# Kernel optimization log

Measured on AMD Instinct MI355X. Metric: run time of the kernel, lower is better.

The kernel has to match this reference:

```python
import jax, jax.numpy as jnp
import numpy as np

B, Q, P, H, W = 4, 64, 32, 512, 512
IDENTITY_ALPHA_EPSILON = 0.001


def setup_inputs() -> dict:
    key = jax.random.key(0)
    k1, k2, k3, k4, k5 = jax.random.split(key, 5)
    patch_alpha = jax.random.uniform(k1, (B, Q, P, P), dtype=jnp.float32)            # sigmoid-like in [0,1]
    centers = jax.random.uniform(k2, (B, Q, 2), dtype=jnp.float32) * 2.0 - 1.0       # tanh range
    depth = jax.random.uniform(k3, (B, Q, 1), dtype=jnp.float32) * 5.0               # sigmoid*5
    sizes = jax.random.uniform(k4, (B, Q, 2), dtype=jnp.float32) * 0.08 + 0.015      # sigmoid*0.08+0.015
    depth_scale = jax.random.uniform(k5, (B, Q, 1), dtype=jnp.float32)
    return {"patch_alpha": patch_alpha, "centers": centers, "depth": depth,
            "sizes": sizes, "depth_scale": depth_scale}


def _grid_sample_bilinear_zeros(img, ix, iy):
    # img: [N,h,w]; ix,iy: pixel coords [N,H,W]; bilinear, zero padding, align_corners=True
    h, w = img.shape[-2], img.shape[-1]
    x0f = jnp.floor(ix)
    y0f = jnp.floor(iy)
    wx = ix - x0f
    wy = iy - y0f
    x0 = x0f.astype(jnp.int32)
    y0 = y0f.astype(jnp.int32)
    n_idx = jnp.arange(img.shape[0])[:, None, None]

    def gather(yc, xc):
        valid = (xc >= 0) & (xc < w) & (yc >= 0) & (yc < h)
        v = img[n_idx, jnp.clip(yc, 0, h - 1), jnp.clip(xc, 0, w - 1)]
        return v * valid.astype(img.dtype)

    v00 = gather(y0, x0)
    v01 = gather(y0, x0 + 1)
    v10 = gather(y0 + 1, x0)
    v11 = gather(y0 + 1, x0 + 1)
    return (v00 * (1 - wx) * (1 - wy) + v01 * wx * (1 - wy)
            + v10 * (1 - wx) * wy + v11 * wx * wy)


def reference(patch_alpha, centers, depth, sizes, depth_scale):
    b, q, ph, pw = patch_alpha.shape
    ys = jnp.linspace(-1.0, 1.0, H)
    xs = jnp.linspace(-1.0, 1.0, W)
    gy, gx = jnp.meshgrid(ys, xs, indexing='ij')                    # [H,W]
    cx = centers[..., 0][:, :, None, None]
    cy = centers[..., 1][:, :, None, None]
    sx = sizes[..., 0][:, :, None, None]
    sy = sizes[..., 1][:, :, None, None]
    lx = jnp.clip((gx - cx) / sx, -1.1, 1.1)                        # [B,Q,H,W]
    ly = jnp.clip((gy - cy) / sy, -1.1, 1.1)
    # normalized -> pixel coords (align_corners=True)
    ix = (lx + 1.0) * 0.5 * (pw - 1)
    iy = (ly + 1.0) * 0.5 * (ph - 1)
    sampled = _grid_sample_bilinear_zeros(
        patch_alpha.reshape(b * q, ph, pw),
        ix.reshape(b * q, H, W), iy.reshape(b * q, H, W)).reshape(b, q, H, W)

    # depth sort, far -> near (descending)
    order = jnp.argsort(-depth[..., 0], axis=1)                      # [B,Q]
    sorted_alpha = jnp.take_along_axis(sampled, order[:, :, None, None], axis=1)
    sorted_depth = jnp.take_along_axis(depth[..., 0], order, axis=1) # [B,Q]
    ident_vals = (order + 1).astype(sampled.dtype)                   # [B,Q]

    # transmittance recurrence as exclusive cumprod of (1-alpha)
    t = jnp.cumprod(1.0 - sorted_alpha, axis=1)                      # [B,Q,H,W]
    t_excl = jnp.concatenate([jnp.ones_like(t[:, :1]), t[:, :-1]], axis=1)
    contrib = sorted_alpha * t_excl                                  # alpha * T before this query

    rendered_depth = jnp.sum(contrib * sorted_depth[:, :, None, None], axis=1)  # [B,H,W]

    hit = contrib > IDENTITY_ALPHA_EPSILON
    first = jnp.argmax(hit, axis=1)                                  # first query (in sorted order) to assign
    any_hit = jnp.any(hit, axis=1)
    identity = ident_vals[jnp.arange(b)[:, None, None], first]       # [B,H,W]
    rendered_identity = jnp.where(any_hit, identity, jnp.zeros((), sampled.dtype))

    occ = jnp.clip(1.0 - t[:, -1], 0.0, 1.0)                         # [B,H,W]
    vis = (occ > 0.05).astype(sampled.dtype)
    rendered_identity = rendered_identity * vis
    rendered_depth = rendered_depth * vis
    rendered_depth = rendered_depth[:, None] * jnp.mean(depth_scale, axis=1, keepdims=True)[..., None]
    return rendered_identity, rendered_depth, occ[:, None]
```

## Files before the change

### kernel.cpp

```cpp
#include <hip/hip_runtime.h>

#define QN 64
#define PATCH 32
#define HH 512
#define WW 512
#define NPIX (4 * 512 * 512)

__global__ __launch_bounds__(256) void render_kernel(
    const float* __restrict__ patch,
    const float* __restrict__ centers,
    const float* __restrict__ depth,
    const float* __restrict__ sizes,
    const float* __restrict__ dscale,
    float* __restrict__ out)
{
#pragma clang fp contract(off)
    const int tid = threadIdx.x;
    const int b   = blockIdx.z;
    const int tx0 = blockIdx.x << 5;
    const int ty0 = blockIdx.y << 5;
    const int xp  = tx0 + ((tid & 7) << 2);
    const int y   = ty0 + (tid >> 3);

    __shared__ float sp[QN][8];
    __shared__ int   slist[QN];
    __shared__ int   scount;
    __shared__ float smean;

    const float STEP = 2.0f / 511.0f;

    if (tid < QN) {
        const int gi = (b << 6) + tid;
        const float d   = depth[gi];
        const float cx0 = centers[gi * 2 + 0];
        const float cy0 = centers[gi * 2 + 1];
        const float sx0 = sizes[gi * 2 + 0];
        const float sy0 = sizes[gi * 2 + 1];

        int rank = 0;
#pragma unroll
        for (int j = 0; j < QN; ++j) {
            const float dj = __shfl(d, j);
            rank += ((dj > d) || ((dj == d) && (j < tid))) ? 1 : 0;
        }
        sp[rank][0] = cx0;
        sp[rank][1] = cy0;
        sp[rank][2] = sx0;
        sp[rank][3] = sy0;
        sp[rank][4] = d;
        sp[rank][5] = (float)(tid + 1);
        sp[rank][6] = __int_as_float(tid);

        float v = dscale[gi];
        for (int off = 32; off; off >>= 1) v += __shfl_down(v, off);
        if (tid == 0) smean = v * (1.0f / 64.0f);

        const float gx_lo = -1.0f + (float)tx0 * STEP;
        const float gx_hi = -1.0f + (float)(tx0 + 31) * STEP;
        const float gy_lo = -1.0f + (float)ty0 * STEP;
        const float gy_hi = -1.0f + (float)(ty0 + 31) * STEP;
        const float C = 1.0660f;
        const float cx = sp[tid][0], cy = sp[tid][1];
        const float sxv = sp[tid][2], syv = sp[tid][3];
        const bool keep = (cx + C * sxv >= gx_lo) && (cx - C * sxv <= gx_hi) &&
                          (cy + C * syv >= gy_lo) && (cy - C * syv <= gy_hi);
        const unsigned long long m = __ballot(keep);
        if (keep) slist[__popcll(m & ((1ull << tid) - 1ull))] = tid;
        if (tid == 0) scount = (int)__popcll(m);
    }
    __syncthreads();

    const int cnt = scount;
    const float gy = -1.0f + (float)y * STEP;
    float gx[4];
#pragma unroll
    for (int k = 0; k < 4; ++k) gx[k] = -1.0f + (float)(xp + k) * STEP;

    float tr[4]  = {1.0f, 1.0f, 1.0f, 1.0f};
    float dp[4]  = {0.0f, 0.0f, 0.0f, 0.0f};
    float idv[4] = {0.0f, 0.0f, 0.0f, 0.0f};
    int hitm = 0;

    for (int i = 0; i < cnt; ++i) {
        const int q = slist[i];
        const float cx  = sp[q][0], cy  = sp[q][1];
        const float sxv = sp[q][2], syv = sp[q][3];
        const float dq  = sp[q][4], iv  = sp[q][5];
        const int   pq  = __float_as_int(sp[q][6]);
        const float* pp = patch + (((size_t)((b << 6) + pq)) << 10);

        float ly = (gy - cy) / syv;
        ly = fminf(fmaxf(ly, -1.1f), 1.1f);
        const float iy  = (ly + 1.0f) * 0.5f * 31.0f;
        const float y0f = floorf(iy);
        const float wy  = iy - y0f;
        const int   yi  = (int)y0f;
        const bool yok0 = (yi >= 0) && (yi < PATCH);
        const bool yok1 = (yi + 1 >= 0) && (yi + 1 < PATCH);
        const int row0 = yi << 5, row1 = (yi + 1) << 5;

#pragma unroll
        for (int k = 0; k < 4; ++k) {
            float lx = (gx[k] - cx) / sxv;
            lx = fminf(fmaxf(lx, -1.1f), 1.1f);
            const float ixf = (lx + 1.0f) * 0.5f * 31.0f;
            const float x0f = floorf(ixf);
            const float wx  = ixf - x0f;
            const int   xi  = (int)x0f;
            const bool xok0 = (xi >= 0) && (xi < PATCH);
            const bool xok1 = (xi + 1 >= 0) && (xi + 1 < PATCH);
            const float v00 = (xok0 && yok0) ? pp[row0 + xi] : 0.0f;
            const float v01 = (xok1 && yok0) ? pp[row0 + xi + 1] : 0.0f;
            const float v10 = (xok0 && yok1) ? pp[row1 + xi] : 0.0f;
            const float v11 = (xok1 && yok1) ? pp[row1 + xi + 1] : 0.0f;

            const float a = v00 * (1.0f - wx) * (1.0f - wy)
                          + v01 * wx * (1.0f - wy)
                          + v10 * (1.0f - wx) * wy
                          + v11 * wx * wy;

            const float contrib = a * tr[k];
            if (!(hitm & (1 << k)) && (contrib > 0.001f)) { hitm |= (1 << k); idv[k] = iv; }
            dp[k] += contrib * dq;
            tr[k] *= (1.0f - a);
        }
    }

    const float sm = smean;
    float4 o_id, o_dp, o_oc;
#pragma unroll
    for (int k = 0; k < 4; ++k) {
        float occ = 1.0f - tr[k];
        occ = fminf(fmaxf(occ, 0.0f), 1.0f);
        const float vis = (occ > 0.05f) ? 1.0f : 0.0f;
        ((float*)&o_id)[k] = idv[k] * vis;
        ((float*)&o_dp)[k] = (dp[k] * vis) * sm;
        ((float*)&o_oc)[k] = occ;
    }

    const size_t pix = ((size_t)b * HH + (size_t)y) * WW + (size_t)xp;
    *(float4*)(out + pix)                    = o_id;
    *(float4*)(out + (size_t)NPIX + pix)     = o_dp;
    *(float4*)(out + 2 * (size_t)NPIX + pix) = o_oc;
}

extern "C" void kernel_launch(void* const* d_in, const int* in_sizes, int n_in,
                              void* d_out, int out_size, void* d_ws, size_t ws_size,
                              hipStream_t stream) {
    const float* patch   = (const float*)d_in[0];
    const float* centers = (const float*)d_in[1];
    const float* depth   = (const float*)d_in[2];
    const float* sizes   = (const float*)d_in[3];
    const float* dscale  = (const float*)d_in[4];
    float* out = (float*)d_out;

    dim3 grid(WW / 32, HH / 32, 4);
    render_kernel<<<grid, 256, 0, stream>>>(patch, centers, depth, sizes, dscale, out);
}
```

Measured before the change: 15.48 us.

## Sort and cull queries per wavefront in registers, removing shared memory and barrier

Every wavefront now loads the 64 query parameters, ranks them by depth, and reorders them into depth order with ds_permute, where before one wave did this and staged the results in shared memory. Culling runs per wave against its own 8-row strip rather than the whole 32x32 tile, giving tighter query lists, and the render loop walks the ballot mask and fetches parameters with shuffles. This drops the __syncthreads and the LDS traffic, at the cost of doing the ranking work once per wave instead of once per block.

```diff
diff --git a/kernel.cpp b/kernel.cpp
--- a/kernel.cpp
+++ b/kernel.cpp
@@ -15,62 +15,51 @@
     float* __restrict__ out)
 {
 #pragma clang fp contract(off)
-    const int tid = threadIdx.x;
-    const int b   = blockIdx.z;
-    const int tx0 = blockIdx.x << 5;
-    const int ty0 = blockIdx.y << 5;
-    const int xp  = tx0 + ((tid & 7) << 2);
-    const int y   = ty0 + (tid >> 3);
-
-    __shared__ float sp[QN][8];
-    __shared__ int   slist[QN];
-    __shared__ int   scount;
-    __shared__ float smean;
+    const int tid  = threadIdx.x;
+    const int lane = tid & 63;
+    const int wv   = tid >> 6;
+    const int b    = blockIdx.z;
+    const int tx0  = blockIdx.x << 5;
+    const int ty0  = blockIdx.y << 5;
+    const int xp   = tx0 + ((lane & 7) << 2);
+    const int y    = ty0 + (wv << 3) + (lane >> 3);
 
     const float STEP = 2.0f / 511.0f;
 
-    if (tid < QN) {
-        const int gi = (b << 6) + tid;
-        const float d   = depth[gi];
-        const float cx0 = centers[gi * 2 + 0];
-        const float cy0 = centers[gi * 2 + 1];
-        const float sx0 = sizes[gi * 2 + 0];
-        const float sy0 = sizes[gi * 2 + 1];
+    const int gi = (b << 6) + lane;
+    const float  d  = depth[gi];
+    const float2 c2 = ((const float2*)centers)[gi];
+    const float2 s2 = ((const float2*)sizes)[gi];
 
-        int rank = 0;
+    float v = dscale[gi];
 #pragma unroll
-        for (int j = 0; j < QN; ++j) {
-            const float dj = __shfl(d, j);
-            rank += ((dj > d) || ((dj == d) && (j < tid))) ? 1 : 0;
-        }
-        sp[rank][0] = cx0;
-        sp[rank][1] = cy0;
-        sp[rank][2] = sx0;
-        sp[rank][3] = sy0;
-        sp[rank][4] = d;
-        sp[rank][5] = (float)(tid + 1);
-        sp[rank][6] = __int_as_float(tid);
+    for (int off = 32; off; off >>= 1) v += __shfl_xor(v, off);
+    const float sm = v * (1.0f / 64.0f);
 
-        float v = dscale[gi];
-        for (int off = 32; off; off >>= 1) v += __shfl_down(v, off);
-        if (tid == 0) smean = v * (1.0f / 64.0f);
+    int rank = 0;
+#pragma unroll
+    for (int j = 0; j < QN; ++j) {
+        const float dj = __shfl(d, j);
+        rank += ((dj > d) || ((dj == d) && (j < lane))) ? 1 : 0;
+    }
 
-        const float gx_lo = -1.0f + (float)tx0 * STEP;
-        const float gx_hi = -1.0f + (float)(tx0 + 31) * STEP;
-        const float gy_lo = -1.0f + (float)ty0 * STEP;
-        const float gy_hi = -1.0f + (float)(ty0 + 31) * STEP;
-        const float C = 1.0660f;
-        const float cx = sp[tid][0], cy = sp[tid][1];
-        const float sxv = sp[tid][2], syv = sp[tid][3];
-        const bool keep = (cx + C * sxv >= gx_lo) && (cx - C * sxv <= gx_hi) &&
-                          (cy + C * syv >= gy_lo) && (cy - C * syv <= gy_hi);
-        const unsigned long long m = __ballot(keep);
-        if (keep) slist[__popcll(m & ((1ull << tid) - 1ull))] = tid;
-        if (tid == 0) scount = (int)__popcll(m);
-    }
-    __syncthreads();
+    const int addr = rank << 2;
+    const float scx = __int_as_float(__builtin_amdgcn_ds_permute(addr, __float_as_int(c2.x)));
+    const float scy = __int_as_float(__builtin_amdgcn_ds_permute(addr, __float_as_int(c2.y)));
+    const float ssx = __int_as_float(__builtin_amdgcn_ds_permute(addr, __float_as_int(s2.x)));
+    const float ssy = __int_as_float(__builtin_amdgcn_ds_permute(addr, __float_as_int(s2.y)));
+    const float sd  = __int_as_float(__builtin_amdgcn_ds_permute(addr, __float_as_int(d)));
+    const int   spq = __builtin_amdgcn_ds_permute(addr, lane);
 
-    const int cnt = scount;
+    const float C = 1.0660f;
+    const float gx_lo = -1.0f + (float)tx0 * STEP;
+    const float gx_hi = -1.0f + (float)(tx0 + 31) * STEP;
+    const float gy_lo = -1.0f + (float)(ty0 + (wv << 3)) * STEP;
+    const float gy_hi = -1.0f + (float)(ty0 + (wv << 3) + 7) * STEP;
+    const bool keep = (scx + C * ssx >= gx_lo) && (scx - C * ssx <= gx_hi) &&
+                      (scy + C * ssy >= gy_lo) && (scy - C * ssy <= gy_hi);
+    unsigned long long m = __ballot(keep);
+
     const float gy = -1.0f + (float)y * STEP;
     float gx[4];
 #pragma unroll
@@ -81,12 +70,16 @@
     float idv[4] = {0.0f, 0.0f, 0.0f, 0.0f};
     int hitm = 0;
 
-    for (int i = 0; i < cnt; ++i) {
-        const int q = slist[i];
-        const float cx  = sp[q][0], cy  = sp[q][1];
-        const float sxv = sp[q][2], syv = sp[q][3];
-        const float dq  = sp[q][4], iv  = sp[q][5];
-        const int   pq  = __float_as_int(sp[q][6]);
+    while (m) {
+        const int i = (int)__builtin_ctzll(m);
+        m &= m - 1;
+        const float cx  = __shfl(scx, i);
+        const float cy  = __shfl(scy, i);
+        const float sxv = __shfl(ssx, i);
+        const float syv = __shfl(ssy, i);
+        const float dq  = __shfl(sd,  i);
+        const int   pq  = __shfl(spq, i);
+        const float iv  = (float)(pq + 1);
         const float* pp = patch + (((size_t)((b << 6) + pq)) << 10);
 
         float ly = (gy - cy) / syv;
@@ -126,7 +119,6 @@
         }
     }
 
-    const float sm = smean;
     float4 o_id, o_dp, o_oc;
 #pragma unroll
     for (int k = 0; k < 4; ++k) {
```

Result: slower. 15.96 us (+3.1%).
